# Kernel optimization log

Hardware: AMD Instinct MI355X
Metric: run time of the kernel (lower is better)

## Reference

```python
import jax, jax.numpy as jnp
from jax import lax
import numpy as np
import math

N, T, H, PD = 1024, 32, 256, 256
E, DT, SD = 2 * H, H // 16, 16  # mamba expand, dt_rank, state_dim
TAU = 1.0

def _xavier(k, shape):
    s = math.sqrt(6.0 / (shape[0] + shape[1]))
    return jax.random.uniform(k, shape, minval=-s, maxval=s, dtype=jnp.float32)

def setup_inputs() -> dict:
    key = jax.random.key(0)
    ks = jax.random.split(key, 40)
    adj = (jax.random.uniform(ks[0], (T, N, N)) < 0.02).astype(jnp.float32)
    p = {
        'adj': adj,
        # input SpatialLayer (pos_dim -> H)
        'msg1_w': _xavier(ks[1], (PD, H)), 'msg1_b': jnp.zeros(H),
        'upd1_w': _xavier(ks[2], (PD + H, H)), 'upd1_b': jnp.zeros(H),
        'ln1_g': jnp.ones(H), 'ln1_b': jnp.zeros(H),
        # second SpatialLayer (H -> H)
        'msg2_w': _xavier(ks[3], (H, H)), 'msg2_b': jnp.zeros(H),
        'upd2_w': _xavier(ks[4], (2 * H, H)), 'upd2_b': jnp.zeros(H),
        'ln2_g': jnp.ones(H), 'ln2_b': jnp.zeros(H),
        # MambaBlock
        'mb_ln_g': jnp.ones(H), 'mb_ln_b': jnp.zeros(H),
        'in_w': _xavier(ks[5], (H, 2 * E)), 'in_b': jnp.zeros(2 * E),
        'delta_w': _xavier(ks[6], (E, DT)), 'delta_b': jnp.zeros(DT),
        'dt_w': _xavier(ks[7], (DT, E)), 'dt_b': jnp.zeros(E),
        'Bp_w': _xavier(ks[8], (E, SD)), 'Bp_b': jnp.zeros(SD),
        'Cp_w': _xavier(ks[9], (E, SD)), 'Cp_b': jnp.zeros(SD),
        'A_log': -jnp.exp(0.1 * jax.random.normal(ks[10], (E, SD))),
        'D_vec': jnp.zeros(E),
        'out_w': _xavier(ks[11], (E, H)), 'out_b': jnp.zeros(H),
        # LateEdgeGateHead
        'q_w': _xavier(ks[12], (H, H)), 'k_w': _xavier(ks[13], (H, H)),
        'gate_bias': jnp.float32(-1.0),
    }
    return p

def _layernorm(x, g, b, eps=1e-5):
    mu = jnp.mean(x, -1, keepdims=True)
    var = jnp.mean(jnp.square(x - mu), -1, keepdims=True)
    return (x - mu) / jnp.sqrt(var + eps) * g + b

def _sincos_pe(n, d):
    pos = jnp.arange(n, dtype=jnp.float32)[:, None]
    div = jnp.exp(jnp.arange(0, d, 2, dtype=jnp.float32) * (-math.log(10000.0) / d))
    ang = pos * div  # [n, d/2]
    return jnp.stack([jnp.sin(ang), jnp.cos(ang)], axis=-1).reshape(n, d)

def reference(adj, msg1_w, msg1_b, upd1_w, upd1_b, ln1_g, ln1_b,
              msg2_w, msg2_b, upd2_w, upd2_b, ln2_g, ln2_b,
              mb_ln_g, mb_ln_b, in_w, in_b, delta_w, delta_b, dt_w, dt_b,
              Bp_w, Bp_b, Cp_w, Cp_b, A_log, D_vec, out_w, out_b,
              q_w, k_w, gate_bias):
    pe = _sincos_pe(N, PD)  # [N, PD]
    # --- spatial layer 1 (shared pe across time) ---
    m1 = pe @ msg1_w + msg1_b                                   # [N, H]
    agg1 = jnp.einsum('tij,jh->tih', adj, m1)                   # [T, N, H]
    x = jnp.concatenate([jnp.broadcast_to(pe, (T, N, PD)), agg1], -1)
    x = _layernorm(jax.nn.relu(x @ upd1_w + upd1_b), ln1_g, ln1_b)
    # --- spatial layer 2 ---
    m2 = x @ msg2_w + msg2_b
    agg2 = jnp.einsum('tij,tjh->tih', adj, m2)
    x = jnp.concatenate([x, agg2], -1)
    x = _layernorm(jax.nn.relu(x @ upd2_w + upd2_b), ln2_g, ln2_b)  # [T, N, H]
    # --- Mamba over time, batch = nodes ---
    seq = jnp.transpose(x, (1, 0, 2))                           # [N, T, H]
    res = seq
    xn = _layernorm(seq, mb_ln_g, mb_ln_b)
    xp = xn @ in_w + in_b
    x1, gate = jnp.split(xp, 2, axis=-1)                        # [N, T, E] each
    x1 = jax.nn.silu(x1)
    delta = jax.nn.softplus((x1 @ delta_w + delta_b) @ dt_w + dt_b)  # [N, T, E]
    Bm = x1 @ Bp_w + Bp_b                                       # [N, T, SD]
    Cm = x1 @ Cp_w + Cp_b
    A = -jnp.exp(A_log)                                         # [E, SD]
    def step(h, inp):
        xt, dt_, bt, ct = inp                                   # [N,E],[N,E],[N,SD],[N,SD]
        A_disc = jnp.exp(dt_[:, :, None] * A)                   # [N, E, SD]
        h = A_disc * h + dt_[:, :, None] * bt[:, None, :] * xt[:, :, None]
        yt = jnp.sum(ct[:, None, :] * h, -1)                    # [N, E]
        return h, yt
    h0 = jnp.zeros((N, E, SD), dtype=seq.dtype)
    xs = (jnp.swapaxes(x1, 0, 1), jnp.swapaxes(delta, 0, 1),
          jnp.swapaxes(Bm, 0, 1), jnp.swapaxes(Cm, 0, 1))
    _, ys = lax.scan(step, h0, xs)                              # [T, N, E]
    y = jnp.swapaxes(ys, 0, 1) + x1 * D_vec
    y = y * jax.nn.silu(gate)
    mb_out = y @ out_w + out_b + res                            # [N, T, H]
    outs = jnp.transpose(mb_out, (1, 0, 2))                     # [T, N, H]
    # --- late gate head per timestep ---
    q = outs @ q_w
    k = outs @ k_w
    scores = jnp.einsum('tnh,tmh->tnm', q, k) / (math.sqrt(H) * max(TAU, 1e-6))
    logits = scores + gate_bias
    probs = jax.nn.sigmoid(logits)
    return outs, probs, logits
```

## Files before the change

### kernel.cpp

```cpp
#include <hip/hip_runtime.h>
#include <hip/hip_bf16.h>

typedef __hip_bfloat16 bf16;
typedef short s16x8 __attribute__((ext_vector_type(8)));
typedef float f32x4 __attribute__((ext_vector_type(4)));

#define T_  32
#define N_  1024
#define H_  256
#define E_  512
#define SD_ 16

static const long MBYTE = 1024L * 1024L;

__device__ __forceinline__ float b2f(bf16 v){ return __bfloat162float(v); }
__device__ __forceinline__ bf16  f2b(float v){ return __float2bfloat16(v); }

#define G2L16(gp, lp) __builtin_amdgcn_global_load_lds( \
    (const __attribute__((address_space(1))) void*)(const void*)(gp), \
    (__attribute__((address_space(3))) void*)(void*)(lp), 16, 0, 0)

struct TDesc { const float* src; int K; int N; bf16* dst; int ldT; };
struct PrepArgs {
    TDesc t[13];
    bf16* pe;
    const float* pa; const float* pb; const float* pc; float* po;
    const float* adj; unsigned short* IDX; int* CNT;
};

__global__ __launch_bounds__(256) void prep_kernel(PrepArgs P){
    int z = blockIdx.z;
    int tid = threadIdx.x;
    if (z < 13) {
        const TDesc d = P.t[z];
        int k0 = blockIdx.x * 32, n0 = blockIdx.y * 32;
        if (k0 >= d.K || n0 >= d.N) return;
        __shared__ float S[32][33];
        int r = tid >> 3, c4 = (tid & 7) * 4;
        #pragma unroll
        for (int u = 0; u < 4; ++u) {
            int k = k0 + r, n = n0 + c4 + u;
            S[r][c4 + u] = (k < d.K && n < d.N) ? d.src[(long)k * d.N + n] : 0.0f;
        }
        __syncthreads();
        int n = n0 + (tid >> 3);
        #pragma unroll
        for (int u = 0; u < 4; ++u) {
            int k = k0 + (tid & 7) * 4 + u;
            if (n < d.N && k < d.K) d.dst[(long)n * d.ldT + k] = f2b(S[(tid & 7) * 4 + u][tid >> 3]);
        }
    } else if (z == 13) {
        int n = blockIdx.y * 32 + blockIdx.x;
        int dd = tid;
        int i2 = (dd >> 1) * 2;
        float div = __expf((float)i2 * (-9.210340371976184f / 256.0f));
        float ang = (float)n * div;
        P.pe[n * 256 + dd] = f2b((dd & 1) ? __cosf(ang) : __sinf(ang));
    } else if (z == 14) {
        if (blockIdx.x || blockIdx.y) return;
        if (tid < 16) P.po[tid] = P.pa[tid];
        else if (tid < 32) P.po[tid] = P.pb[tid - 16];
        else if (tid < 48) P.po[tid] = P.pc[tid - 32];
    } else {
        int r = (z - 15) * 1024 + blockIdx.y * 32 + blockIdx.x;
        const float* arow = P.adj + ((long)r << 10);
        __shared__ int wcnt[4];
        int wv = tid >> 6, lane = tid & 63;
        int total = 0;
        unsigned short* out = P.IDX + (long)r * 128;
        #pragma unroll
        for (int u = 0; u < 4; ++u) {
            float av = arow[u * 256 + tid];
            unsigned long long mask = __ballot(av != 0.0f);
            if (lane == 0) wcnt[wv] = __popcll(mask);
            __syncthreads();
            int base = total;
            for (int w2 = 0; w2 < wv; ++w2) base += wcnt[w2];
            if (av != 0.0f) {
                int pos = base + __popcll(mask & ((1ull << lane) - 1ull));
                if (pos < 128) out[pos] = (unsigned short)(u * 256 + tid);
            }
            total += wcnt[0] + wcnt[1] + wcnt[2] + wcnt[3];
            __syncthreads();
        }
        if (tid == 0) P.CNT[r] = total < 128 ? total : 128;
    }
}

template<int OP>
__global__ __launch_bounds__(256) void mfma_gemm128(
    const bf16* __restrict__ A, int lda,
    const bf16* BT0, const bf16* BT1, int ldbt0, int ldbt1,
    float* Cf0, float* Cf1, bf16* Cb0, bf16* Cb1, int ldc,
    int K, const float* bias0, const float* bias1, const float* res)
{
    int z = blockIdx.z;
    const bf16* BT = z ? BT1 : BT0;
    int ldbt = z ? ldbt1 : ldbt0;
    float* Cf = z ? Cf1 : Cf0;
    bf16*  Cb = z ? Cb1 : Cb0;
    const float* bias = z ? bias1 : bias0;

    __shared__ short As[4096];
    __shared__ short Bs[4096];
    int tid = threadIdx.x;
    int w = tid >> 6, l = tid & 63;
    int wr = w >> 1, wc = w & 1;
    long row0 = (long)blockIdx.y * 128, col0 = (long)blockIdx.x * 128;
    const short* Ag = (const short*)A + row0 * lda;
    const short* Bg = (const short*)BT + col0 * ldbt;
    int sr = w * 16 + (l >> 2);
    int sc = (l & 3) * 8;
    short* lA = As + w * 512 + l * 8;
    short* lB = Bs + w * 512 + l * 8;
    f32x4 acc[4][4] = {};
    for (int k0 = 0; k0 < K; k0 += 32) {
        G2L16(Ag + (long)sr * lda + k0 + sc, lA);
        G2L16(Ag + (long)(sr + 64) * lda + k0 + sc, lA + 2048);
        G2L16(Bg + (long)sr * ldbt + k0 + sc, lB);
        G2L16(Bg + (long)(sr + 64) * ldbt + k0 + sc, lB + 2048);
        __syncthreads();
        s16x8 af[4], bf[4];
        #pragma unroll
        for (int f = 0; f < 4; ++f) {
            af[f] = *(const s16x8*)&As[(wr * 64 + f * 16 + (l & 15)) * 32 + (l >> 4) * 8];
            bf[f] = *(const s16x8*)&Bs[(wc * 64 + f * 16 + (l & 15)) * 32 + (l >> 4) * 8];
        }
        #pragma unroll
        for (int fm = 0; fm < 4; ++fm)
            #pragma unroll
            for (int fn = 0; fn < 4; ++fn)
                acc[fm][fn] = __builtin_amdgcn_mfma_f32_16x16x32_bf16(af[fm], bf[fn], acc[fm][fn], 0, 0, 0);
        __syncthreads();
    }
    #pragma unroll
    for (int fm = 0; fm < 4; ++fm) {
        int er = (int)row0 + wr * 64 + fm * 16 + (l >> 4) * 4;
        #pragma unroll
        for (int fn = 0; fn < 4; ++fn) {
            int ec = (int)col0 + wc * 64 + fn * 16 + (l & 15);
            float bb = bias ? bias[ec] : 0.0f;
            #pragma unroll
            for (int rg = 0; rg < 4; ++rg) {
                long idx = (long)(er + rg) * ldc + ec;
                float v = acc[fm][fn][rg] + bb;
                if (res) v += res[idx];
                if (OP == 1) v = v / (1.0f + __expf(-v));
                if (Cf) Cf[idx] = v;
                if (Cb) Cb[idx] = f2b(v);
            }
        }
    }
}

__global__ __launch_bounds__(256) void score_mfma128(
    const bf16* __restrict__ Q, const bf16* __restrict__ Km,
    float* __restrict__ probs, float* __restrict__ logits,
    const float* __restrict__ gbp)
{
    int t = blockIdx.z;
    const short* Ag = (const short*)(Q  + (long)t * N_ * 256) + (long)blockIdx.y * 128 * 256;
    const short* Bg = (const short*)(Km + (long)t * N_ * 256) + (long)blockIdx.x * 128 * 256;
    __shared__ short As[4096];
    __shared__ short Bs[4096];
    int tid = threadIdx.x;
    int w = tid >> 6, l = tid & 63;
    int wr = w >> 1, wc = w & 1;
    int sr = w * 16 + (l >> 2);
    int sc = (l & 3) * 8;
    short* lA = As + w * 512 + l * 8;
    short* lB = Bs + w * 512 + l * 8;
    f32x4 acc[4][4] = {};
    for (int k0 = 0; k0 < 256; k0 += 32) {
        G2L16(Ag + (long)sr * 256 + k0 + sc, lA);
        G2L16(Ag + (long)(sr + 64) * 256 + k0 + sc, lA + 2048);
        G2L16(Bg + (long)sr * 256 + k0 + sc, lB);
        G2L16(Bg + (long)(sr + 64) * 256 + k0 + sc, lB + 2048);
        __syncthreads();
        s16x8 af[4], bf[4];
        #pragma unroll
        for (int f = 0; f < 4; ++f) {
            af[f] = *(const s16x8*)&As[(wr * 64 + f * 16 + (l & 15)) * 32 + (l >> 4) * 8];
            bf[f] = *(const s16x8*)&Bs[(wc * 64 + f * 16 + (l & 15)) * 32 + (l >> 4) * 8];
        }
        #pragma unroll
        for (int fm = 0; fm < 4; ++fm)
            #pragma unroll
            for (int fn = 0; fn < 4; ++fn)
                acc[fm][fn] = __builtin_amdgcn_mfma_f32_16x16x32_bf16(af[fm], bf[fn], acc[fm][fn], 0, 0, 0);
        __syncthreads();
    }
    float gb = gbp[0];
    long tbase = (long)t * N_ * N_;
    int row0 = blockIdx.y * 128, col0 = blockIdx.x * 128;
    #pragma unroll
    for (int fm = 0; fm < 4; ++fm) {
        int er = row0 + wr * 64 + fm * 16 + (l >> 4) * 4;
        #pragma unroll
        for (int fn = 0; fn < 4; ++fn) {
            int ec = col0 + wc * 64 + fn * 16 + (l & 15);
            #pragma unroll
            for (int rg = 0; rg < 4; ++rg) {
                float zz = acc[fm][fn][rg] * 0.0625f + gb;
                long idx = tbase + (long)(er + rg) * N_ + ec;
                __builtin_nontemporal_store(zz, &logits[idx]);
                __builtin_nontemporal_store(1.0f / (1.0f + __expf(-zz)), &probs[idx]);
            }
        }
    }
}

__global__ __launch_bounds__(256) void mfma_gemm64(
    const bf16* __restrict__ A, int lda,
    const bf16* __restrict__ BT, int ldbt,
    float* __restrict__ Cf, int ldc,
    int M, int N, int K, const float* __restrict__ bias)
{
    __shared__ short As[64][40];
    __shared__ short Bs[64][40];
    int tid = threadIdx.x;
    int w = tid >> 6, l = tid & 63;
    int row0 = blockIdx.y * 64, col0 = blockIdx.x * 64;
    int sr = tid >> 2, sk = (tid & 3) * 8;
    const short* Ag = (const short*)A;
    const short* Bg = (const short*)BT;
    f32x4 acc[4] = {};
    for (int k0 = 0; k0 < K; k0 += 32) {
        *(s16x8*)&As[sr][sk] = *(const s16x8*)(Ag + (long)(row0 + sr) * lda + k0 + sk);
        int bn = col0 + sr;
        s16x8 bv = {};
        if (bn < N) bv = *(const s16x8*)(Bg + (long)bn * ldbt + k0 + sk);
        *(s16x8*)&Bs[sr][sk] = bv;
        __syncthreads();
        s16x8 a = *(const s16x8*)&As[w * 16 + (l & 15)][(l >> 4) * 8];
        #pragma unroll
        for (int ct = 0; ct < 4; ++ct) {
            s16x8 b = *(const s16x8*)&Bs[ct * 16 + (l & 15)][(l >> 4) * 8];
            acc[ct] = __builtin_amdgcn_mfma_f32_16x16x32_bf16(a, b, acc[ct], 0, 0, 0);
        }
        __syncthreads();
    }
    int er = row0 + w * 16 + (l >> 4) * 4;
    int ec = l & 15;
    #pragma unroll
    for (int ct = 0; ct < 4; ++ct) {
        int gc = col0 + ct * 16 + ec;
        if (gc >= N) continue;
        float bb = bias ? bias[gc] : 0.0f;
        #pragma unroll
        for (int rg = 0; rg < 4; ++rg)
            Cf[(long)(er + rg) * ldc + gc] = acc[ct][rg] + bb;
    }
}

__global__ __launch_bounds__(256) void agg_gather(
    const unsigned short* __restrict__ IDX, const int* __restrict__ CNT,
    const bf16* __restrict__ Bm, long tstride,
    bf16* __restrict__ out, int old, int ooff)
{
    int r = blockIdx.x;
    int t = r >> 10;
    const bf16* B = Bm + (long)t * tstride;
    __shared__ unsigned short sidx[128];
    int tid = threadIdx.x;
    int cnt = CNT[r];
    if (tid < 128) sidx[tid] = IDX[(long)r * 128 + tid];
    __syncthreads();
    float a0 = 0.0f, a1 = 0.0f, a2 = 0.0f, a3 = 0.0f;
    int k = 0;
    for (; k + 4 <= cnt; k += 4) {
        float v0 = b2f(B[(long)sidx[k]     * 256 + tid]);
        float v1 = b2f(B[(long)sidx[k + 1] * 256 + tid]);
        float v2 = b2f(B[(long)sidx[k + 2] * 256 + tid]);
        float v3 = b2f(B[(long)sidx[k + 3] * 256 + tid]);
        a0 += v0; a1 += v1; a2 += v2; a3 += v3;
    }
    for (; k < cnt; ++k) a0 += b2f(B[(long)sidx[k] * 256 + tid]);
    out[(long)r * old + ooff + tid] = f2b((a0 + a1) + (a2 + a3));
}

__global__ __launch_bounds__(256) void row_ln1(
    const float* __restrict__ in, const float* __restrict__ addf,
    const float* __restrict__ g, const float* __restrict__ b,
    bf16* __restrict__ out, int rows)
{
    int wv = threadIdx.x >> 6, lane = threadIdx.x & 63;
    int row = blockIdx.x * 4 + wv;
    if (row >= rows) return;
    const float* p = in + (long)row * 256 + lane * 4;
    const float* q = addf + (long)(row & 1023) * 256 + lane * 4;
    float v[4];
    #pragma unroll
    for (int u = 0; u < 4; ++u) v[u] = fmaxf(p[u] + q[u], 0.0f);
    float s = v[0] + v[1] + v[2] + v[3];
    #pragma unroll
    for (int o = 32; o >= 1; o >>= 1) s += __shfl_xor(s, o, 64);
    float mu = s * (1.0f / 256.0f);
    float d0 = v[0]-mu, d1 = v[1]-mu, d2 = v[2]-mu, d3 = v[3]-mu;
    float sq = d0*d0 + d1*d1 + d2*d2 + d3*d3;
    #pragma unroll
    for (int o = 32; o >= 1; o >>= 1) sq += __shfl_xor(sq, o, 64);
    float rs = rsqrtf(sq * (1.0f / 256.0f) + 1e-5f);
    bf16* o = out + (long)row * 512 + lane * 4;
    #pragma unroll
    for (int u = 0; u < 4; ++u)
        o[u] = f2b((v[u] - mu) * rs * g[lane * 4 + u] + b[lane * 4 + u]);
}

__global__ __launch_bounds__(256) void dbl_ln(
    const float* __restrict__ in,
    const float* __restrict__ g2, const float* __restrict__ b2,
    const float* __restrict__ gm, const float* __restrict__ bm,
    float* __restrict__ X2f, bf16* __restrict__ XNb, int rows)
{
    int wv = threadIdx.x >> 6, lane = threadIdx.x & 63;
    int row = blockIdx.x * 4 + wv;
    if (row >= rows) return;
    const float* p = in + (long)row * 256 + lane * 4;
    float v[4];
    #pragma unroll
    for (int u = 0; u < 4; ++u) v[u] = fmaxf(p[u], 0.0f);
    float s = v[0] + v[1] + v[2] + v[3];
    #pragma unroll
    for (int o = 32; o >= 1; o >>= 1) s += __shfl_xor(s, o, 64);
    float mu = s * (1.0f / 256.0f);
    float sq = 0.0f;
    #pragma unroll
    for (int u = 0; u < 4; ++u) { float d = v[u] - mu; sq += d * d; }
    #pragma unroll
    for (int o = 32; o >= 1; o >>= 1) sq += __shfl_xor(sq, o, 64);
    float rs = rsqrtf(sq * (1.0f / 256.0f) + 1e-5f);
    float o1[4];
    float* qx = X2f + (long)row * 256 + lane * 4;
    #pragma unroll
    for (int u = 0; u < 4; ++u) {
        o1[u] = (v[u] - mu) * rs * g2[lane * 4 + u] + b2[lane * 4 + u];
        qx[u] = o1[u];
    }
    float s2 = o1[0] + o1[1] + o1[2] + o1[3];
    #pragma unroll
    for (int o = 32; o >= 1; o >>= 1) s2 += __shfl_xor(s2, o, 64);
    float mu2 = s2 * (1.0f / 256.0f);
    float sq2 = 0.0f;
    #pragma unroll
    for (int u = 0; u < 4; ++u) { float d = o1[u] - mu2; sq2 += d * d; }
    #pragma unroll
    for (int o = 32; o >= 1; o >>= 1) sq2 += __shfl_xor(sq2, o, 64);
    float rs2 = rsqrtf(sq2 * (1.0f / 256.0f) + 1e-5f);
    bf16* qn = XNb + (long)row * 256 + lane * 4;
    #pragma unroll
    for (int u = 0; u < 4; ++u)
        qn[u] = f2b((o1[u] - mu2) * rs2 * gm[lane * 4 + u] + bm[lane * 4 + u]);
}

__global__ __launch_bounds__(512) void scan2(
    const bf16* __restrict__ X1,
    bf16* __restrict__ G,
    const float* __restrict__ DBC,
    const bf16* __restrict__ DTwT,
    const float* __restrict__ DTb,
    const float* __restrict__ A_log,
    const float* __restrict__ D_vec)
{
    int n = blockIdx.x;
    int e = threadIdx.x;
    float A[SD_], wdt[SD_];
    #pragma unroll
    for (int s = 0; s < SD_; ++s) A[s] = -__expf(A_log[e * SD_ + s]);
    #pragma unroll
    for (int s = 0; s < SD_; ++s) wdt[s] = b2f(DTwT[e * SD_ + s]);
    float dtb = DTb[e];
    float Dv = D_vec[e];
    float h[SD_];
    #pragma unroll
    for (int s = 0; s < SD_; ++s) h[s] = 0.0f;
    for (int t = 0; t < T_; ++t) {
        long row = (long)t * N_ + n;
        const float* dbc = DBC + row * 48;
        float z = dtb;
        #pragma unroll
        for (int k = 0; k < SD_; ++k) z += dbc[k] * wdt[k];
        float dt = (z > 15.0f) ? z : __logf(1.0f + __expf(z));
        float x1 = b2f(X1[row * (long)E_ + e]);
        float gv = b2f(G[row * (long)E_ + e]);
        float dx = dt * x1;
        float yv = 0.0f;
        #pragma unroll
        for (int s = 0; s < SD_; ++s) {
            h[s] = __expf(dt * A[s]) * h[s] + dx * dbc[16 + s];
            yv += dbc[32 + s] * h[s];
        }
        G[row * (long)E_ + e] = f2b((yv + x1 * Dv) * gv);
    }
}

extern "C" void kernel_launch(void* const* d_in, const int* in_sizes, int n_in,
                              void* d_out, int out_size, void* d_ws, size_t ws_size,
                              hipStream_t stream)
{
    if (ws_size < (size_t)(212 * MBYTE)) return;
    if (n_in != 32 || in_sizes[0] != T_ * N_ * N_ || in_sizes[15] != 256 * 1024) return;

    const float* adj = (const float*)d_in[0];
    const float* P1w = (const float*)d_in[1];
    const float* P1b = (const float*)d_in[2];
    const float* U1w = (const float*)d_in[3];
    const float* U1b = (const float*)d_in[4];
    const float* L1g = (const float*)d_in[5];
    const float* L1b = (const float*)d_in[6];
    const float* P2w = (const float*)d_in[7];
    const float* P2b = (const float*)d_in[8];
    const float* U2w = (const float*)d_in[9];
    const float* U2b = (const float*)d_in[10];
    const float* L2g = (const float*)d_in[11];
    const float* L2b = (const float*)d_in[12];
    const float* MBg = (const float*)d_in[13];
    const float* MBb = (const float*)d_in[14];
    const float* INw = (const float*)d_in[15];
    const float* INb = (const float*)d_in[16];
    const float* DLw = (const float*)d_in[17];
    const float* DLb = (const float*)d_in[18];
    const float* DTw = (const float*)d_in[19];
    const float* DTb = (const float*)d_in[20];
    const float* BPw = (const float*)d_in[21];
    const float* BPb = (const float*)d_in[22];
    const float* CPw = (const float*)d_in[23];
    const float* CPb = (const float*)d_in[24];
    const float* ALg = (const float*)d_in[25];
    const float* DV  = (const float*)d_in[26];
    const float* OWw = (const float*)d_in[27];
    const float* OWb = (const float*)d_in[28];
    const float* QWw = (const float*)d_in[29];
    const float* KWw = (const float*)d_in[30];
    const float* GB  = (const float*)d_in[31];

    char* w = (char*)d_ws;
    float* R0    = (float*)(w + 0);
    bf16*  XCATb = (bf16*)(w + 32 * MBYTE);
    bf16*  AGG1b = (bf16*)(w + 64 * MBYTE);
    bf16*  M2b   = (bf16*)(w + 64 * MBYTE);
    bf16*  OUTb  = (bf16*)(w + 64 * MBYTE);
    bf16*  X1b   = (bf16*)(w + 80 * MBYTE);
    bf16*  Gb    = (bf16*)(w + 112 * MBYTE);
    float* X2f   = (float*)(w + 144 * MBYTE);
    bf16*  Qb    = (bf16*)(w + 144 * MBYTE);
    bf16*  Kb    = (bf16*)(w + 160 * MBYTE);
    bf16*  XNb   = (bf16*)(w + 176 * MBYTE);
    float* DBC   = (float*)(w + 192 * MBYTE);
    unsigned short* IDX = (unsigned short*)(w + 198 * MBYTE);
    int*   CNT   = (int*)(w + 206 * MBYTE);
    float* BASE1 = (float*)(w + 207 * MBYTE);
    bf16*  PEb   = (bf16*)(w + 208 * MBYTE);
    bf16*  M1b   = (bf16*)(w + 208 * MBYTE + 524288);
    bf16*  WT    = (bf16*)(w + 209 * MBYTE);
    float* B48   = (float*)(w + 211 * MBYTE);

    bf16* P1wT  = WT + 0;
    bf16* U1wT  = WT + 65536;
    bf16* P2wT  = WT + 196608;
    bf16* U2wT  = WT + 262144;
    bf16* INwT  = WT + 393216;
    bf16* DTwT  = WT + 655360;
    bf16* OWwT  = WT + 663552;
    bf16* QWwT  = WT + 794624;
    bf16* KWwT  = WT + 860160;
    bf16* DBCwT = WT + 925696;

    float* out0       = (float*)d_out;
    float* out_probs  = out0 + (long)T_ * N_ * H_;
    float* out_logits = out_probs + (long)T_ * N_ * N_;

    const int RN = T_ * N_;
    dim3 blk(256);
    const float* fnull = nullptr;
    float* f32null = nullptr;
    bf16*  b16null = nullptr;

    PrepArgs P;
    P.t[0]  = {P1w, 256, 256,  P1wT, 256};
    P.t[1]  = {U1w, 512, 256,  U1wT, 512};
    P.t[2]  = {P2w, 256, 256,  P2wT, 256};
    P.t[3]  = {U2w, 512, 256,  U2wT, 512};
    P.t[4]  = {INw, 256, 1024, INwT, 256};
    P.t[5]  = {DTw, 16,  512,  DTwT, 16};
    P.t[6]  = {OWw, 512, 256,  OWwT, 512};
    P.t[7]  = {QWw, 256, 256,  QWwT, 256};
    P.t[8]  = {KWw, 256, 256,  KWwT, 256};
    P.t[9]  = {DLw, 512, 16,   DBCwT, 512};
    P.t[10] = {BPw, 512, 16,   DBCwT + 16 * 512, 512};
    P.t[11] = {CPw, 512, 16,   DBCwT + 32 * 512, 512};
    P.t[12] = {DLw, 1,   1,    DBCwT, 512};
    P.pe = PEb; P.pa = DLb; P.pb = BPb; P.pc = CPb; P.po = B48;
    P.adj = adj; P.IDX = IDX; P.CNT = CNT;
    hipLaunchKernelGGL(prep_kernel, dim3(32, 32, 47), blk, 0, stream, P);

    hipLaunchKernelGGL((mfma_gemm128<0>), dim3(2, 8, 2), blk, 0, stream,
                       PEb, 256, P1wT, U1wT, 256, 512,
                       f32null, BASE1, M1b, b16null, 256, 256, P1b, U1b, fnull);

    hipLaunchKernelGGL(agg_gather, dim3(RN), blk, 0, stream, IDX, CNT, M1b, 0L, AGG1b, 256, 0);

    hipLaunchKernelGGL((mfma_gemm128<0>), dim3(2, 256, 1), blk, 0, stream,
                       AGG1b, 256, U1wT + 256, U1wT + 256, 512, 512,
                       R0, f32null, b16null, b16null, 256, 256, fnull, fnull, fnull);
    hipLaunchKernelGGL(row_ln1, dim3(RN / 4), blk, 0, stream, R0, BASE1, L1g, L1b, XCATb, RN);

    hipLaunchKernelGGL((mfma_gemm128<0>), dim3(2, 256, 1), blk, 0, stream,
                       XCATb, 512, P2wT, P2wT, 256, 256,
                       f32null, f32null, M2b, b16null, 256, 256, P2b, fnull, fnull);

    hipLaunchKernelGGL(agg_gather, dim3(RN), blk, 0, stream, IDX, CNT, M2b,
                       (long)N_ * 256, XCATb, 512, 256);

    hipLaunchKernelGGL((mfma_gemm128<0>), dim3(2, 256, 1), blk, 0, stream,
                       XCATb, 512, U2wT, U2wT, 512, 512,
                       R0, f32null, b16null, b16null, 256, 512, U2b, fnull, fnull);
    hipLaunchKernelGGL(dbl_ln, dim3(RN / 4), blk, 0, stream,
                       R0, L2g, L2b, MBg, MBb, X2f, XNb, RN);

    hipLaunchKernelGGL((mfma_gemm128<1>), dim3(4, 256, 2), blk, 0, stream,
                       XNb, 256, INwT, INwT + 512 * 256, 256, 256,
                       f32null, f32null, X1b, Gb, 512, 256, INb, INb + 512, fnull);

    hipLaunchKernelGGL(mfma_gemm64, dim3(1, 512), blk, 0, stream,
                       X1b, 512, DBCwT, 512, DBC, 48, RN, 48, 512, B48);

    hipLaunchKernelGGL(scan2, dim3(N_), dim3(512), 0, stream,
                       X1b, Gb, DBC, DTwT, DTb, ALg, DV);

    hipLaunchKernelGGL((mfma_gemm128<0>), dim3(2, 256, 1), blk, 0, stream,
                       Gb, 512, OWwT, OWwT, 512, 512,
                       out0, f32null, OUTb, b16null, 256, 512, OWb, fnull, X2f);

    hipLaunchKernelGGL((mfma_gemm128<0>), dim3(2, 256, 2), blk, 0, stream,
                       OUTb, 256, QWwT, KWwT, 256, 256,
                       f32null, f32null, Qb, Kb, 256, 256, fnull, fnull, fnull);

    hipLaunchKernelGGL(score_mfma128, dim3(8, 8, T_), blk, 0, stream,
                       Qb, Kb, out_probs, out_logits, GB);
}
```

Before: 565.2 us.

## Fuse LayerNorm epilogues into full-row GEMM kernels and store residual in bf16

Adds a GEMM kernel in which each block computes 64 full rows of 256 output columns, so the ReLU+LayerNorm (and the double LayerNorm) can run in the epilogue through cross-wave reductions in shared memory. This replaces two GEMM+row_ln kernel pairs and removes the fp32 R0 round trip through global memory. It also stores the residual X2 in bf16 instead of fp32, which halves its traffic but adds rounding to the residual. The new kernel launches fewer blocks (512) and runs extra syncthreads-heavy reductions, so GEMM efficiency may drop.

```diff
diff --git a/kernel.cpp b/kernel.cpp
--- a/kernel.cpp
+++ b/kernel.cpp
@@ -92,7 +92,7 @@
     const bf16* __restrict__ A, int lda,
     const bf16* BT0, const bf16* BT1, int ldbt0, int ldbt1,
     float* Cf0, float* Cf1, bf16* Cb0, bf16* Cb1, int ldc,
-    int K, const float* bias0, const float* bias1, const float* res)
+    int K, const float* bias0, const float* bias1, const bf16* resb)
 {
     int z = blockIdx.z;
     const bf16* BT = z ? BT1 : BT0;
@@ -144,10 +144,179 @@
             for (int rg = 0; rg < 4; ++rg) {
                 long idx = (long)(er + rg) * ldc + ec;
                 float v = acc[fm][fn][rg] + bb;
-                if (res) v += res[idx];
+                if (resb) v += b2f(resb[idx]);
                 if (OP == 1) v = v / (1.0f + __expf(-v));
                 if (Cf) Cf[idx] = v;
                 if (Cb) Cb[idx] = f2b(v);
+            }
+        }
+    }
+}
+
+template<bool DBL>
+__global__ __launch_bounds__(256) void mfma_gemm_ln(
+    const bf16* __restrict__ A, int lda,
+    const bf16* __restrict__ BT, int ldbt, int K,
+    const float* __restrict__ bias, const float* __restrict__ addf,
+    const float* __restrict__ g1, const float* __restrict__ b1,
+    const float* __restrict__ g2, const float* __restrict__ b2,
+    bf16* __restrict__ O1, int ldo1, int ooff1,
+    bf16* __restrict__ O2)
+{
+    __shared__ short As[2048];
+    __shared__ short Bs[8192];
+    __shared__ float part[4][64];
+    int tid = threadIdx.x;
+    int w = tid >> 6, l = tid & 63;
+    long row0 = (long)blockIdx.x * 64;
+    const short* Ag = (const short*)A + row0 * lda;
+    const short* Bg = (const short*)BT;
+    int srA = w * 16 + (l >> 2);
+    int sc = (l & 3) * 8;
+    short* lA = As + w * 512 + l * 8;
+    short* lB = Bs + w * 512 + l * 8;
+    f32x4 acc[4][4] = {};
+    for (int k0 = 0; k0 < K; k0 += 32) {
+        G2L16(Ag + (long)srA * lda + k0 + sc, lA);
+        #pragma unroll
+        for (int p = 0; p < 4; ++p)
+            G2L16(Bg + (long)(p * 64 + srA) * ldbt + k0 + sc, lB + p * 2048);
+        __syncthreads();
+        s16x8 af[4], bf[4];
+        #pragma unroll
+        for (int f = 0; f < 4; ++f) {
+            af[f] = *(const s16x8*)&As[(f * 16 + (l & 15)) * 32 + (l >> 4) * 8];
+            bf[f] = *(const s16x8*)&Bs[(w * 64 + f * 16 + (l & 15)) * 32 + (l >> 4) * 8];
+        }
+        #pragma unroll
+        for (int fm = 0; fm < 4; ++fm)
+            #pragma unroll
+            for (int fn = 0; fn < 4; ++fn)
+                acc[fm][fn] = __builtin_amdgcn_mfma_f32_16x16x32_bf16(af[fm], bf[fn], acc[fm][fn], 0, 0, 0);
+        __syncthreads();
+    }
+    #pragma unroll
+    for (int fm = 0; fm < 4; ++fm) {
+        int rb = fm * 16 + (l >> 4) * 4;
+        #pragma unroll
+        for (int fn = 0; fn < 4; ++fn) {
+            int ec = w * 64 + fn * 16 + (l & 15);
+            float bb = bias ? bias[ec] : 0.0f;
+            #pragma unroll
+            for (int rg = 0; rg < 4; ++rg) {
+                float v = acc[fm][fn][rg] + bb;
+                if (addf) v += addf[(long)((row0 + rb + rg) & 1023) * 256 + ec];
+                acc[fm][fn][rg] = fmaxf(v, 0.0f);
+            }
+        }
+    }
+    float mu[4][4], rs[4][4];
+    #pragma unroll
+    for (int fm = 0; fm < 4; ++fm)
+        #pragma unroll
+        for (int rg = 0; rg < 4; ++rg) {
+            float s = acc[fm][0][rg] + acc[fm][1][rg] + acc[fm][2][rg] + acc[fm][3][rg];
+            #pragma unroll
+            for (int o = 8; o >= 1; o >>= 1) s += __shfl_xor(s, o, 64);
+            if ((l & 15) == 0) part[w][fm * 16 + (l >> 4) * 4 + rg] = s;
+            mu[fm][rg] = s;
+        }
+    __syncthreads();
+    #pragma unroll
+    for (int fm = 0; fm < 4; ++fm)
+        #pragma unroll
+        for (int rg = 0; rg < 4; ++rg) {
+            int r = fm * 16 + (l >> 4) * 4 + rg;
+            mu[fm][rg] = (part[0][r] + part[1][r] + part[2][r] + part[3][r]) * (1.0f / 256.0f);
+        }
+    __syncthreads();
+    #pragma unroll
+    for (int fm = 0; fm < 4; ++fm)
+        #pragma unroll
+        for (int rg = 0; rg < 4; ++rg) {
+            float s = 0.0f;
+            #pragma unroll
+            for (int fn = 0; fn < 4; ++fn) { float d = acc[fm][fn][rg] - mu[fm][rg]; s += d * d; }
+            #pragma unroll
+            for (int o = 8; o >= 1; o >>= 1) s += __shfl_xor(s, o, 64);
+            if ((l & 15) == 0) part[w][fm * 16 + (l >> 4) * 4 + rg] = s;
+        }
+    __syncthreads();
+    #pragma unroll
+    for (int fm = 0; fm < 4; ++fm)
+        #pragma unroll
+        for (int rg = 0; rg < 4; ++rg) {
+            int r = fm * 16 + (l >> 4) * 4 + rg;
+            float var = (part[0][r] + part[1][r] + part[2][r] + part[3][r]) * (1.0f / 256.0f);
+            rs[fm][rg] = rsqrtf(var + 1e-5f);
+        }
+    #pragma unroll
+    for (int fm = 0; fm < 4; ++fm) {
+        int rb = fm * 16 + (l >> 4) * 4;
+        #pragma unroll
+        for (int fn = 0; fn < 4; ++fn) {
+            int ec = w * 64 + fn * 16 + (l & 15);
+            float gg = g1[ec], bbb = b1[ec];
+            #pragma unroll
+            for (int rg = 0; rg < 4; ++rg) {
+                float o1 = (acc[fm][fn][rg] - mu[fm][rg]) * rs[fm][rg] * gg + bbb;
+                acc[fm][fn][rg] = o1;
+                O1[(long)(row0 + rb + rg) * ldo1 + ooff1 + ec] = f2b(o1);
+            }
+        }
+    }
+    if (DBL) {
+        __syncthreads();
+        #pragma unroll
+        for (int fm = 0; fm < 4; ++fm)
+            #pragma unroll
+            for (int rg = 0; rg < 4; ++rg) {
+                float s = acc[fm][0][rg] + acc[fm][1][rg] + acc[fm][2][rg] + acc[fm][3][rg];
+                #pragma unroll
+                for (int o = 8; o >= 1; o >>= 1) s += __shfl_xor(s, o, 64);
+                if ((l & 15) == 0) part[w][fm * 16 + (l >> 4) * 4 + rg] = s;
+            }
+        __syncthreads();
+        #pragma unroll
+        for (int fm = 0; fm < 4; ++fm)
+            #pragma unroll
+            for (int rg = 0; rg < 4; ++rg) {
+                int r = fm * 16 + (l >> 4) * 4 + rg;
+                mu[fm][rg] = (part[0][r] + part[1][r] + part[2][r] + part[3][r]) * (1.0f / 256.0f);
+            }
+        __syncthreads();
+        #pragma unroll
+        for (int fm = 0; fm < 4; ++fm)
+            #pragma unroll
+            for (int rg = 0; rg < 4; ++rg) {
+                float s = 0.0f;
+                #pragma unroll
+                for (int fn = 0; fn < 4; ++fn) { float d = acc[fm][fn][rg] - mu[fm][rg]; s += d * d; }
+                #pragma unroll
+                for (int o = 8; o >= 1; o >>= 1) s += __shfl_xor(s, o, 64);
+                if ((l & 15) == 0) part[w][fm * 16 + (l >> 4) * 4 + rg] = s;
+            }
+        __syncthreads();
+        #pragma unroll
+        for (int fm = 0; fm < 4; ++fm)
+            #pragma unroll
+            for (int rg = 0; rg < 4; ++rg) {
+                int r = fm * 16 + (l >> 4) * 4 + rg;
+                float var = (part[0][r] + part[1][r] + part[2][r] + part[3][r]) * (1.0f / 256.0f);
+                rs[fm][rg] = rsqrtf(var + 1e-5f);
+            }
+        #pragma unroll
+        for (int fm = 0; fm < 4; ++fm) {
+            int rb = fm * 16 + (l >> 4) * 4;
+            #pragma unroll
+            for (int fn = 0; fn < 4; ++fn) {
+                int ec = w * 64 + fn * 16 + (l & 15);
+                float gg = g2[ec], bbb = b2[ec];
+                #pragma unroll
+                for (int rg = 0; rg < 4; ++rg) {
+                    float o2 = (acc[fm][fn][rg] - mu[fm][rg]) * rs[fm][rg] * gg + bbb;
+                    O2[(long)(row0 + rb + rg) * 256 + ec] = f2b(o2);
+                }
             }
         }
     }
@@ -277,80 +446,6 @@
     }
     for (; k < cnt; ++k) a0 += b2f(B[(long)sidx[k] * 256 + tid]);
     out[(long)r * old + ooff + tid] = f2b((a0 + a1) + (a2 + a3));
-}
-
-__global__ __launch_bounds__(256) void row_ln1(
-    const float* __restrict__ in, const float* __restrict__ addf,
-    const float* __restrict__ g, const float* __restrict__ b,
-    bf16* __restrict__ out, int rows)
-{
-    int wv = threadIdx.x >> 6, lane = threadIdx.x & 63;
-    int row = blockIdx.x * 4 + wv;
-    if (row >= rows) return;
-    const float* p = in + (long)row * 256 + lane * 4;
-    const float* q = addf + (long)(row & 1023) * 256 + lane * 4;
-    float v[4];
-    #pragma unroll
-    for (int u = 0; u < 4; ++u) v[u] = fmaxf(p[u] + q[u], 0.0f);
-    float s = v[0] + v[1] + v[2] + v[3];
-    #pragma unroll
-    for (int o = 32; o >= 1; o >>= 1) s += __shfl_xor(s, o, 64);
-    float mu = s * (1.0f / 256.0f);
-    float d0 = v[0]-mu, d1 = v[1]-mu, d2 = v[2]-mu, d3 = v[3]-mu;
-    float sq = d0*d0 + d1*d1 + d2*d2 + d3*d3;
-    #pragma unroll
-    for (int o = 32; o >= 1; o >>= 1) sq += __shfl_xor(sq, o, 64);
-    float rs = rsqrtf(sq * (1.0f / 256.0f) + 1e-5f);
-    bf16* o = out + (long)row * 512 + lane * 4;
-    #pragma unroll
-    for (int u = 0; u < 4; ++u)
-        o[u] = f2b((v[u] - mu) * rs * g[lane * 4 + u] + b[lane * 4 + u]);
-}
-
-__global__ __launch_bounds__(256) void dbl_ln(
-    const float* __restrict__ in,
-    const float* __restrict__ g2, const float* __restrict__ b2,
-    const float* __restrict__ gm, const float* __restrict__ bm,
-    float* __restrict__ X2f, bf16* __restrict__ XNb, int rows)
-{
-    int wv = threadIdx.x >> 6, lane = threadIdx.x & 63;
-    int row = blockIdx.x * 4 + wv;
-    if (row >= rows) return;
-    const float* p = in + (long)row * 256 + lane * 4;
-    float v[4];
-    #pragma unroll
-    for (int u = 0; u < 4; ++u) v[u] = fmaxf(p[u], 0.0f);
-    float s = v[0] + v[1] + v[2] + v[3];
-    #pragma unroll
-    for (int o = 32; o >= 1; o >>= 1) s += __shfl_xor(s, o, 64);
-    float mu = s * (1.0f / 256.0f);
-    float sq = 0.0f;
-    #pragma unroll
-    for (int u = 0; u < 4; ++u) { float d = v[u] - mu; sq += d * d; }
-    #pragma unroll
-    for (int o = 32; o >= 1; o >>= 1) sq += __shfl_xor(sq, o, 64);
-    float rs = rsqrtf(sq * (1.0f / 256.0f) + 1e-5f);
-    float o1[4];
-    float* qx = X2f + (long)row * 256 + lane * 4;
-    #pragma unroll
-    for (int u = 0; u < 4; ++u) {
-        o1[u] = (v[u] - mu) * rs * g2[lane * 4 + u] + b2[lane * 4 + u];
-        qx[u] = o1[u];
-    }
-    float s2 = o1[0] + o1[1] + o1[2] + o1[3];
-    #pragma unroll
-    for (int o = 32; o >= 1; o >>= 1) s2 += __shfl_xor(s2, o, 64);
-    float mu2 = s2 * (1.0f / 256.0f);
-    float sq2 = 0.0f;
-    #pragma unroll
-    for (int u = 0; u < 4; ++u) { float d = o1[u] - mu2; sq2 += d * d; }
-    #pragma unroll
-    for (int o = 32; o >= 1; o >>= 1) sq2 += __shfl_xor(sq2, o, 64);
-    float rs2 = rsqrtf(sq2 * (1.0f / 256.0f) + 1e-5f);
-    bf16* qn = XNb + (long)row * 256 + lane * 4;
-    #pragma unroll
-    for (int u = 0; u < 4; ++u)
-        qn[u] = f2b((o1[u] - mu2) * rs2 * gm[lane * 4 + u] + bm[lane * 4 + u]);
 }
 
 __global__ __launch_bounds__(512) void scan2(
@@ -442,7 +537,6 @@
     bf16*  OUTb  = (bf16*)(w + 64 * MBYTE);
     bf16*  X1b   = (bf16*)(w + 80 * MBYTE);
     bf16*  Gb    = (bf16*)(w + 112 * MBYTE);
-    float* X2f   = (float*)(w + 144 * MBYTE);
     bf16*  Qb    = (bf16*)(w + 144 * MBYTE);
     bf16*  Kb    = (bf16*)(w + 160 * MBYTE);
     bf16*  XNb   = (bf16*)(w + 176 * MBYTE);
@@ -454,6 +548,7 @@
     bf16*  M1b   = (bf16*)(w + 208 * MBYTE + 524288);
     bf16*  WT    = (bf16*)(w + 209 * MBYTE);
     float* B48   = (float*)(w + 211 * MBYTE);
+    bf16*  X2b   = (bf16*)(w + 0);
 
     bf16* P1wT  = WT + 0;
     bf16* U1wT  = WT + 65536;
@@ -475,6 +570,7 @@
     const float* fnull = nullptr;
     float* f32null = nullptr;
     bf16*  b16null = nullptr;
+    const bf16* cb16null = nullptr;
 
     PrepArgs P;
     P.t[0]  = {P1w, 256, 256,  P1wT, 256};
@@ -496,31 +592,30 @@
 
     hipLaunchKernelGGL((mfma_gemm128<0>), dim3(2, 8, 2), blk, 0, stream,
                        PEb, 256, P1wT, U1wT, 256, 512,
-                       f32null, BASE1, M1b, b16null, 256, 256, P1b, U1b, fnull);
+                       f32null, BASE1, M1b, b16null, 256, 256, P1b, U1b, cb16null);
 
     hipLaunchKernelGGL(agg_gather, dim3(RN), blk, 0, stream, IDX, CNT, M1b, 0L, AGG1b, 256, 0);
 
-    hipLaunchKernelGGL((mfma_gemm128<0>), dim3(2, 256, 1), blk, 0, stream,
-                       AGG1b, 256, U1wT + 256, U1wT + 256, 512, 512,
-                       R0, f32null, b16null, b16null, 256, 256, fnull, fnull, fnull);
-    hipLaunchKernelGGL(row_ln1, dim3(RN / 4), blk, 0, stream, R0, BASE1, L1g, L1b, XCATb, RN);
+    hipLaunchKernelGGL((mfma_gemm_ln<false>), dim3(RN / 64), blk, 0, stream,
+                       AGG1b, 256, U1wT + 256, 512, 256,
+                       fnull, BASE1, L1g, L1b, fnull, fnull,
+                       XCATb, 512, 0, b16null);
 
     hipLaunchKernelGGL((mfma_gemm128<0>), dim3(2, 256, 1), blk, 0, stream,
                        XCATb, 512, P2wT, P2wT, 256, 256,
-                       f32null, f32null, M2b, b16null, 256, 256, P2b, fnull, fnull);
+                       f32null, f32null, M2b, b16null, 256, 256, P2b, fnull, cb16null);
 
     hipLaunchKernelGGL(agg_gather, dim3(RN), blk, 0, stream, IDX, CNT, M2b,
                        (long)N_ * 256, XCATb, 512, 256);
 
-    hipLaunchKernelGGL((mfma_gemm128<0>), dim3(2, 256, 1), blk, 0, stream,
-                       XCATb, 512, U2wT, U2wT, 512, 512,
-                       R0, f32null, b16null, b16null, 256, 512, U2b, fnull, fnull);
-    hipLaunchKernelGGL(dbl_ln, dim3(RN / 4), blk, 0, stream,
-                       R0, L2g, L2b, MBg, MBb, X2f, XNb, RN);
+    hipLaunchKernelGGL((mfma_gemm_ln<true>), dim3(RN / 64), blk, 0, stream,
+                       XCATb, 512, U2wT, 512, 512,
+                       U2b, fnull, L2g, L2b, MBg, MBb,
+                       X2b, 256, 0, XNb);
 
     hipLaunchKernelGGL((mfma_gemm128<1>), dim3(4, 256, 2), blk, 0, stream,
                        XNb, 256, INwT, INwT + 512 * 256, 256, 256,
-                       f32null, f32null, X1b, Gb, 512, 256, INb, INb + 512, fnull);
+                       f32null, f32null, X1b, Gb, 512, 256, INb, INb + 512, cb16null);
 
     hipLaunchKernelGGL(mfma_gemm64, dim3(1, 512), blk, 0, stream,
                        X1b, 512, DBCwT, 512, DBC, 48, RN, 48, 512, B48);
@@ -530,11 +625,11 @@
 
     hipLaunchKernelGGL((mfma_gemm128<0>), dim3(2, 256, 1), blk, 0, stream,
                        Gb, 512, OWwT, OWwT, 512, 512,
-                       out0, f32null, OUTb, b16null, 256, 512, OWb, fnull, X2f);
+                       out0, f32null, OUTb, b16null, 256, 512, OWb, fnull, X2b);
 
     hipLaunchKernelGGL((mfma_gemm128<0>), dim3(2, 256, 2), blk, 0, stream,
                        OUTb, 256, QWwT, KWwT, 256, 256,
-                       f32null, f32null, Qb, Kb, 256, 256, fnull, fnull, fnull);
+                       f32null, f32null, Qb, Kb, 256, 256, fnull, fnull, cb16null);
 
     hipLaunchKernelGGL(score_mfma128, dim3(8, 8, T_), blk, 0, stream,
                        Qb, Kb, out_probs, out_logits, GB);
```

Result: slower. 666.7 us (+18.0%).
